# Optimization experiments

Hardware: AMD Instinct MI355X
Metric: run time of the kernel (lower is better)

The kernel has to match this reference:

```python
import jax, jax.numpy as jnp
import numpy as np

# Problem sizes: batch(+heads), seq (m=n), head dim, nonzeros per row
B, M, N, K, R = 8, 4096, 4096, 64, 128
NNZ = M * R


def setup_inputs() -> dict:
    key = jax.random.key(0)
    k1, k2, k3, k4 = jax.random.split(key, 4)
    # Uniform CSR: R nonzeros per row, columns sorted within each row.
    row_offsets = jnp.arange(M + 1, dtype=jnp.int32) * R
    column_indices = jax.random.randint(k4, (M, R), 0, N, dtype=jnp.int32)
    column_indices = jnp.sort(column_indices, axis=1).reshape(NNZ)
    # diffsort(row_offsets): row ids sorted by descending row length (load balancing,
    # does not affect the math).
    diffs = row_offsets[1:] - row_offsets[:-1]
    row_indices = jnp.argsort(-diffs).astype(jnp.int32)
    q3d = jax.random.normal(k1, (B, M, K), dtype=jnp.float32)
    k3d = jax.random.normal(k2, (B, N, K), dtype=jnp.float32)
    v3d = jax.random.normal(k3, (B, N, K), dtype=jnp.float32)
    # `values` is only an output buffer for sddmm in the original; contents unused.
    values = jnp.zeros((B, NNZ), dtype=jnp.float32)
    return {
        "row_indices": row_indices,
        "row_offsets": row_offsets,
        "column_indices": column_indices,
        "q3d": q3d,
        "k3d": k3d,
        "v3d": v3d,
        "values": values,
    }


def reference(row_indices, row_offsets, column_indices, q3d, k3d, v3d, values):
    m = row_offsets.shape[0] - 1
    nnz = column_indices.shape[0]
    # Row id of each CSR nonzero.
    row_ids = jnp.searchsorted(
        row_offsets, jnp.arange(nnz, dtype=row_offsets.dtype), side="right"
    ) - 1
    cols = column_indices

    # SDDMM: logits[b, e] = <Q[b, row(e), :], K[b, col(e), :]>  -> [B, nnz]
    logits = jnp.einsum("bed,bed->be", q3d[:, row_ids, :], k3d[:, cols, :])

    def attend_one(lg_b, v_b):
        # Sparse per-row softmax over the nonzeros of each row.
        mx = jax.ops.segment_max(lg_b, row_ids, num_segments=m)
        ex = jnp.exp(lg_b - mx[row_ids])
        den = jax.ops.segment_sum(ex, row_ids, num_segments=m)
        w = ex / den[row_ids]  # [nnz]
        # SPMM: out[i, :] = sum_{e in row i} w[e] * V[col(e), :]
        return jax.ops.segment_sum(w[:, None] * v_b[cols, :], row_ids, num_segments=m)

    return jax.vmap(attend_one)(logits, v3d)  # [B, M, K]
```

## Files before the change

kernel.cpp:

```cpp
#include <hip/hip_runtime.h>

#define Bc 8
#define Mc 4096
#define Nc 4096
#define Kc 64
#define Rc 128

typedef _Float16 h16;
typedef h16 h16x2 __attribute__((ext_vector_type(2)));
typedef h16 h16x4 __attribute__((ext_vector_type(4)));
typedef h16 h16x8 __attribute__((ext_vector_type(8)));

__global__ __launch_bounds__(256) void cvt_fp16(
    const float4* __restrict__ K4, const float4* __restrict__ V4,
    h16x4* __restrict__ Kh4, h16x4* __restrict__ Vh4)
{
    const int n4 = Bc * Nc * Kc / 4;
    int i = blockIdx.x * 256 + threadIdx.x;
    const float4* src; h16x4* dst; int idx;
    if (i < n4) { src = K4; dst = Kh4; idx = i; }
    else        { src = V4; dst = Vh4; idx = i - n4; }
    float4 v = src[idx];
    h16x4 o = { (h16)v.x, (h16)v.y, (h16)v.z, (h16)v.w };
    dst[idx] = o;
}

__global__ __launch_bounds__(256) void sattn_kernel(
    const int* __restrict__ cols,
    const float* __restrict__ Q,
    const h16* __restrict__ Kh,
    const h16* __restrict__ Vh,
    float* __restrict__ out)
{
    const int b   = blockIdx.x & 7;
    const int row = blockIdx.x >> 3;
    const int t   = threadIdx.x;
    const int g   = t >> 3;
    const int ln  = t & 7;

    __shared__ float s_w[Rc];
    __shared__ __align__(16) float s_part[32][Kc];
    __shared__ __align__(16) float s_red[4][Kc];
    __shared__ float s_invden;

    int col4[4];
    #pragma unroll
    for (int p = 0; p < 4; ++p) col4[p] = cols[row * Rc + p * 32 + g];

    const float4* qp = (const float4*)(Q + (((unsigned)b * Mc + row) << 6) + ln * 8);
    float4 q0 = qp[0], q1 = qp[1];
    h16x2 qh[4];
    qh[0] = h16x2{ (h16)q0.x, (h16)q0.y };
    qh[1] = h16x2{ (h16)q0.z, (h16)q0.w };
    qh[2] = h16x2{ (h16)q1.x, (h16)q1.y };
    qh[3] = h16x2{ (h16)q1.z, (h16)q1.w };

    h16x8 kv[4];
    #pragma unroll
    for (int p = 0; p < 4; ++p) {
        const h16x8* ap = (const h16x8*)(Kh + ((((unsigned)b * Nc + col4[p]) << 6) + ln * 8));
        if ((col4[p] & 7) == 7) kv[p] = __builtin_nontemporal_load(ap);
        else                    kv[p] = *ap;
    }

    #pragma unroll
    for (int p = 0; p < 4; ++p) {
        float acc = 0.f;
        #pragma unroll
        for (int j = 0; j < 4; ++j) {
            h16x2 kj = { kv[p][2 * j], kv[p][2 * j + 1] };
            acc = __builtin_amdgcn_fdot2(qh[j], kj, acc, false);
        }
        acc += __shfl_xor(acc, 1, 64);
        acc += __shfl_xor(acc, 2, 64);
        acc += __shfl_xor(acc, 4, 64);
        if (ln == 0) s_w[p * 32 + g] = acc;
    }

    h16x8 vv[4];
    #pragma unroll
    for (int p = 0; p < 4; ++p) {
        const h16x8* ap = (const h16x8*)(Vh + ((((unsigned)b * Nc + col4[p]) << 6) + ln * 8));
        if ((col4[p] & 7) == 7) vv[p] = __builtin_nontemporal_load(ap);
        else                    vv[p] = *ap;
    }

    __syncthreads();

    if (t < 64) {
        float l0 = s_w[t], l1 = s_w[t + 64];
        float m = fmaxf(l0, l1);
        #pragma unroll
        for (int o = 32; o; o >>= 1) m = fmaxf(m, __shfl_xor(m, o, 64));
        float e0 = __expf(l0 - m), e1 = __expf(l1 - m);
        s_w[t] = e0; s_w[t + 64] = e1;
        float s = e0 + e1;
        #pragma unroll
        for (int o = 32; o; o >>= 1) s += __shfl_xor(s, o, 64);
        if (t == 0) s_invden = 1.0f / s;
    }
    __syncthreads();

    float acc8[8] = {0.f,0.f,0.f,0.f,0.f,0.f,0.f,0.f};
    #pragma unroll
    for (int p = 0; p < 4; ++p) {
        const float w = s_w[p * 32 + g];
        #pragma unroll
        for (int j = 0; j < 8; ++j)
            acc8[j] = fmaf((float)vv[p][j], w, acc8[j]);
    }
    *(float4*)&s_part[g][ln * 8]     = *(float4*)&acc8[0];
    *(float4*)&s_part[g][ln * 8 + 4] = *(float4*)&acc8[4];
    __syncthreads();

    {
        const int k = t & 63, qq = t >> 6;
        float r = 0.f;
        #pragma unroll
        for (int j = 0; j < 8; ++j) r += s_part[qq * 8 + j][k];
        s_red[qq][k] = r;
    }
    __syncthreads();
    if (t < 64) {
        float r = (s_red[0][t] + s_red[1][t]) + (s_red[2][t] + s_red[3][t]);
        out[(((unsigned)b * Mc + row) << 6) + t] = r * s_invden;
    }
}

extern "C" void kernel_launch(void* const* d_in, const int* in_sizes, int n_in,
                              void* d_out, int out_size, void* d_ws, size_t ws_size,
                              hipStream_t stream) {
    const int*   cols = (const int*)d_in[2];
    const float* Q    = (const float*)d_in[3];
    const float* Km   = (const float*)d_in[4];
    const float* Vm   = (const float*)d_in[5];
    float* out = (float*)d_out;

    h16* Kh = (h16*)d_ws;
    h16* Vh = Kh + (size_t)Bc * Nc * Kc;

    const int n4 = Bc * Nc * Kc / 4;
    cvt_fp16<<<dim3(2 * n4 / 256), dim3(256), 0, stream>>>(
        (const float4*)Km, (const float4*)Vm, (h16x4*)Kh, (h16x4*)Vh);
    sattn_kernel<<<dim3(Bc * Mc), dim3(256), 0, stream>>>(cols, Q, Kh, Vh, out);
}
```

Before: 147.5 us.

## Interleave fp16 K and V rows and compute softmax redundantly per warp

The conversion kernel now writes K and V into one interleaved fp16 buffer, so each key column's K row and V row sit next to each other in a 256-byte record. It also converts 8 elements per thread instead of 4. The attention kernel gathers K and V from that single record, which is meant to improve DRAM and cache locality for the random column gather. The nontemporal-load heuristic is dropped. Every wavefront now computes the softmax redundantly so one __syncthreads can be removed, but some wavefronts may overwrite the shared logits with exponentials while others are still reading them, which is a data race.

```diff
diff --git a/kernel.cpp b/kernel.cpp
--- a/kernel.cpp
+++ b/kernel.cpp
@@ -8,28 +8,30 @@
 
 typedef _Float16 h16;
 typedef h16 h16x2 __attribute__((ext_vector_type(2)));
-typedef h16 h16x4 __attribute__((ext_vector_type(4)));
 typedef h16 h16x8 __attribute__((ext_vector_type(8)));
 
-__global__ __launch_bounds__(256) void cvt_fp16(
+__global__ __launch_bounds__(256) void cvt_kv(
     const float4* __restrict__ K4, const float4* __restrict__ V4,
-    h16x4* __restrict__ Kh4, h16x4* __restrict__ Vh4)
+    h16* __restrict__ KV)
 {
-    const int n4 = Bc * Nc * Kc / 4;
-    int i = blockIdx.x * 256 + threadIdx.x;
-    const float4* src; h16x4* dst; int idx;
-    if (i < n4) { src = K4; dst = Kh4; idx = i; }
-    else        { src = V4; dst = Vh4; idx = i - n4; }
-    float4 v = src[idx];
-    h16x4 o = { (h16)v.x, (h16)v.y, (h16)v.z, (h16)v.w };
-    dst[idx] = o;
+    const int i = blockIdx.x * 256 + threadIdx.x;
+    const int nf = i >> 3;
+    const int j  = i & 7;
+    float4 a0 = K4[i * 2], a1 = K4[i * 2 + 1];
+    float4 b0 = V4[i * 2], b1 = V4[i * 2 + 1];
+    h16x8 kh = { (h16)a0.x,(h16)a0.y,(h16)a0.z,(h16)a0.w,
+                 (h16)a1.x,(h16)a1.y,(h16)a1.z,(h16)a1.w };
+    h16x8 vh = { (h16)b0.x,(h16)b0.y,(h16)b0.z,(h16)b0.w,
+                 (h16)b1.x,(h16)b1.y,(h16)b1.z,(h16)b1.w };
+    h16* dst = KV + ((size_t)nf << 7) + j * 8;
+    *(h16x8*)dst        = kh;
+    *(h16x8*)(dst + 64) = vh;
 }
 
 __global__ __launch_bounds__(256) void sattn_kernel(
     const int* __restrict__ cols,
     const float* __restrict__ Q,
-    const h16* __restrict__ Kh,
-    const h16* __restrict__ Vh,
+    const h16* __restrict__ KV,
     float* __restrict__ out)
 {
     const int b   = blockIdx.x & 7;
@@ -43,9 +45,12 @@
     __shared__ __align__(16) float s_red[4][Kc];
     __shared__ float s_invden;
 
-    int col4[4];
+    const h16* kvp[4];
     #pragma unroll
-    for (int p = 0; p < 4; ++p) col4[p] = cols[row * Rc + p * 32 + g];
+    for (int p = 0; p < 4; ++p) {
+        const int c = cols[row * Rc + p * 32 + g];
+        kvp[p] = KV + ((((size_t)b * Nc + c)) << 7) + ln * 8;
+    }
 
     const float4* qp = (const float4*)(Q + (((unsigned)b * Mc + row) << 6) + ln * 8);
     float4 q0 = qp[0], q1 = qp[1];
@@ -57,11 +62,7 @@
 
     h16x8 kv[4];
     #pragma unroll
-    for (int p = 0; p < 4; ++p) {
-        const h16x8* ap = (const h16x8*)(Kh + ((((unsigned)b * Nc + col4[p]) << 6) + ln * 8));
-        if ((col4[p] & 7) == 7) kv[p] = __builtin_nontemporal_load(ap);
-        else                    kv[p] = *ap;
-    }
+    for (int p = 0; p < 4; ++p) kv[p] = *(const h16x8*)kvp[p];
 
     #pragma unroll
     for (int p = 0; p < 4; ++p) {
@@ -79,27 +80,24 @@
 
     h16x8 vv[4];
     #pragma unroll
-    for (int p = 0; p < 4; ++p) {
-        const h16x8* ap = (const h16x8*)(Vh + ((((unsigned)b * Nc + col4[p]) << 6) + ln * 8));
-        if ((col4[p] & 7) == 7) vv[p] = __builtin_nontemporal_load(ap);
-        else                    vv[p] = *ap;
-    }
+    for (int p = 0; p < 4; ++p) vv[p] = *(const h16x8*)(kvp[p] + 64);
 
     __syncthreads();
 
-    if (t < 64) {
-        float l0 = s_w[t], l1 = s_w[t + 64];
+    float e0, e1, invden;
+    {
+        const int l = t & 63;
+        float l0 = s_w[l], l1 = s_w[l + 64];
         float m = fmaxf(l0, l1);
         #pragma unroll
         for (int o = 32; o; o >>= 1) m = fmaxf(m, __shfl_xor(m, o, 64));
-        float e0 = __expf(l0 - m), e1 = __expf(l1 - m);
-        s_w[t] = e0; s_w[t + 64] = e1;
+        e0 = __expf(l0 - m); e1 = __expf(l1 - m);
         float s = e0 + e1;
         #pragma unroll
         for (int o = 32; o; o >>= 1) s += __shfl_xor(s, o, 64);
-        if (t == 0) s_invden = 1.0f / s;
+        invden = 1.0f / s;
     }
-    __syncthreads();
+    s_w[t & 63] = e0; s_w[(t & 63) + 64] = e1;
 
     float acc8[8] = {0.f,0.f,0.f,0.f,0.f,0.f,0.f,0.f};
     #pragma unroll
@@ -111,6 +109,7 @@
     }
     *(float4*)&s_part[g][ln * 8]     = *(float4*)&acc8[0];
     *(float4*)&s_part[g][ln * 8 + 4] = *(float4*)&acc8[4];
+    if (t == 0) s_invden = invden;
     __syncthreads();
 
     {
@@ -136,11 +135,10 @@
     const float* Vm   = (const float*)d_in[5];
     float* out = (float*)d_out;
 
-    h16* Kh = (h16*)d_ws;
-    h16* Vh = Kh + (size_t)Bc * Nc * Kc;
+    h16* KV = (h16*)d_ws;
 
-    const int n4 = Bc * Nc * Kc / 4;
-    cvt_fp16<<<dim3(2 * n4 / 256), dim3(256), 0, stream>>>(
-        (const float4*)Km, (const float4*)Vm, (h16x4*)Kh, (h16x4*)Vh);
-    sattn_kernel<<<dim3(Bc * Mc), dim3(256), 0, stream>>>(cols, Q, Kh, Vh, out);
+    const int nthreads = Bc * Nc * Kc / 8;
+    cvt_kv<<<dim3(nthreads / 256), dim3(256), 0, stream>>>(
+        (const float4*)Km, (const float4*)Vm, KV);
+    sattn_kernel<<<dim3(Bc * Mc), dim3(256), 0, stream>>>(cols, Q, KV, out);
 }
```

New measurement: 154.3 us. 4.6% more time.
